# Kernel optimization log

Measured on AMD Instinct MI355X. Metric: run time of the kernel, lower is better.

## Reference

```python
import jax, jax.numpy as jnp
import numpy as np

DIM = 2048
NUM_HEADS = 16
HEAD_DIM = 128
SEQ = 4096
HDIM = NUM_HEADS * HEAD_DIM
EPS = 1e-6


def _rope_tables(seq_len, head_dim):
    quarter = head_dim // 4
    ang = (1.0 / 1024.0) ** np.linspace(0.0, 1.0, quarter, dtype=np.float32)
    ang = np.concatenate([ang, np.zeros(quarter, dtype=np.float32)])  # [head_dim//2]
    theta = np.arange(seq_len, dtype=np.float32)[:, None] * ang[None, :]  # [T, D/2]
    return jnp.asarray(np.cos(theta)), jnp.asarray(np.sin(theta))


def _rms_norm(x):
    return x * jax.lax.rsqrt(jnp.mean(x * x, axis=-1, keepdims=True) + EPS)


def _apply_rope(x, cos, sin):
    # x: [B, T, H, D]; cos/sin: [T, D/2]
    c = cos[None, :, None, :]
    s = sin[None, :, None, :]
    x1, x2 = jnp.split(x, 2, axis=-1)
    return jnp.concatenate([x1 * c + x2 * s, -x1 * s + x2 * c], axis=-1)


def setup_inputs() -> dict:
    key = jax.random.key(0)
    k1, k2, k3, k4, k5 = jax.random.split(key, 5)
    x = jax.random.normal(k1, (1, SEQ, DIM), dtype=jnp.float32)
    ve = jax.random.normal(k2, (1, SEQ, HDIM), dtype=jnp.float32)
    lambdas = jax.random.uniform(k3, (2,), dtype=jnp.float32)
    bound = (3.0 ** 0.5) * 0.5 * DIM ** (-0.5)
    qkv_w = jax.random.uniform(k4, (3, HDIM, DIM), dtype=jnp.float32, minval=-bound, maxval=bound)
    proj_w = 0.02 * jax.random.normal(k5, (DIM, HDIM), dtype=jnp.float32)
    return {"x": x, "ve": ve, "lambdas": lambdas, "qkv_w": qkv_w, "proj_w": proj_w}


def reference(x, ve, lambdas, qkv_w, proj_w):
    B, T, _ = x.shape
    cos, sin = _rope_tables(T, HEAD_DIM)
    # fused QKV projection: qkv_w [3, hdim, dim]
    qkv = jnp.einsum('btd,ced->cbte', x, qkv_w)  # [3, B, T, hdim]
    q, k, v = [a.reshape(B, T, NUM_HEADS, HEAD_DIM) for a in qkv]
    q = _apply_rope(_rms_norm(q), cos, sin)
    k = _apply_rope(_rms_norm(k), cos, sin)
    v = lambdas[0] * v + lambdas[1] * ve.reshape(v.shape)
    # causal SDPA, default scale 1/sqrt(head_dim)
    scale = 1.0 / jnp.sqrt(jnp.float32(HEAD_DIM))
    scores = jnp.einsum('bthd,bshd->bhts', q, k) * scale  # [B, H, T, T]
    causal = jnp.tril(jnp.ones((T, T), dtype=bool))
    scores = jnp.where(causal[None, None], scores, jnp.float32(-1e30))
    probs = jax.nn.softmax(scores, axis=-1)
    out = jnp.einsum('bhts,bshd->bthd', probs, v).reshape(B, T, HDIM)
    return out @ proj_w.T
```

## Files before the change

### kernel.cpp

```cpp
#include <hip/hip_runtime.h>
#include <cstdint>
#include <cstddef>

constexpr int T_SEQ = 4096;
constexpr int NH    = 16;
constexpr int HD    = 128;
constexpr int DIM   = 2048;
constexpr int HDIM  = 2048;

typedef __attribute__((ext_vector_type(8)))  short  short8;
typedef __attribute__((ext_vector_type(4)))  float  f32x4;
typedef __attribute__((ext_vector_type(16))) float  f32x16;
typedef __attribute__((ext_vector_type(8)))  unsigned short u16x8;
typedef __attribute__((ext_vector_type(4)))  unsigned short u16x4;
typedef __attribute__((ext_vector_type(4)))  unsigned uint4v;
typedef __attribute__((ext_vector_type(2)))  int int2v;

__device__ __forceinline__ unsigned short f2bf(float f) {
  unsigned u = __float_as_uint(f);
  return (unsigned short)((u + 0x7FFFu + ((u >> 16) & 1u)) >> 16);
}
__device__ __forceinline__ float bf2f(unsigned short h) {
  return __uint_as_float(((unsigned)h) << 16);
}
__device__ __forceinline__ void gload_lds16(const void* g, void* l) {
  __builtin_amdgcn_global_load_lds((const __attribute__((address_space(1))) void*)g,
                                   (__attribute__((address_space(3))) void*)l, 16, 0, 0);
}
__device__ __forceinline__ int2v plswap(int a, int b) {
  return __builtin_amdgcn_permlane32_swap(a, b, false, false);
}
__device__ __forceinline__ void bar() {
  asm volatile("" ::: "memory");
  __builtin_amdgcn_s_barrier();
  asm volatile("" ::: "memory");
}
#define VMCNT(n) asm volatile("s_waitcnt vmcnt(" #n ")" ::: "memory")

__global__ __launch_bounds__(256) void prep_all(const float* __restrict__ x,
                                                const float* __restrict__ qkv_w,
                                                const float* __restrict__ proj_w,
                                                unsigned short* __restrict__ xb,
                                                unsigned short* __restrict__ wqb,
                                                unsigned short* __restrict__ pwb,
                                                float* __restrict__ cosT,
                                                float* __restrict__ sinT) {
  constexpr int N1 = T_SEQ * DIM / 4;
  constexpr int N2 = N1 + 3 * HDIM * DIM / 4;
  constexpr int N3 = N2 + DIM * HDIM / 4;
  int gid = blockIdx.x * 256 + threadIdx.x;
  const float* src; unsigned short* dst; int i4;
  if (gid < N1)      { src = x;      dst = xb;  i4 = gid; }
  else if (gid < N2) { src = qkv_w;  dst = wqb; i4 = gid - N1; }
  else if (gid < N3) { src = proj_w; dst = pwb; i4 = gid - N2; }
  else {
    int idx = gid - N3;
    int t = idx >> 6, i = idx & 63;
    float ang = (i < 32) ? exp2f(-10.0f * (float)i / 31.0f) : 0.0f;
    float th = (float)t * ang;
    cosT[idx] = cosf(th);
    sinT[idx] = sinf(th);
    return;
  }
  float4 v = ((const float4*)src)[i4];
  u16x4 o; o.x = f2bf(v.x); o.y = f2bf(v.y); o.z = f2bf(v.z); o.w = f2bf(v.w);
  ((u16x4*)dst)[i4] = o;
}

template <int MODE>
__global__ __launch_bounds__(512) void gemm256(const unsigned short* __restrict__ A,
                                               const unsigned short* __restrict__ B,
                                               int K, unsigned short* __restrict__ outb,
                                               float* __restrict__ outf, int N) {
  __shared__ __align__(16) char SM[3 * 49152];
  const int tid = threadIdx.x, w = tid >> 6, lane = tid & 63;
  const int wm = w >> 2, wn = w & 3;
  const int lr = lane >> 4, lc = lane & 15, lc7 = lc & 7;
  const int cpx = gridDim.x >> 3;
  const int idx = (blockIdx.x & 7) * cpx + (blockIdx.x >> 3);
  const int m0 = (idx & 31) * 128, n0 = (idx >> 5) * 256;

  const int arow = lane >> 3;
  const int xcol = ((lane & 7) ^ ((lane >> 3) & 7)) * 8;

  auto stageA = [&](int buf, int t) {
    char* base = SM + buf * 49152;
#pragma unroll
    for (int i = 0; i < 2; i++) {
      int c = w + i * 8;
      gload_lds16(A + (size_t)(m0 + c * 8 + arow) * K + t * 64 + xcol, base + c * 1024);
    }
  };
  auto stageB0 = [&](int buf, int t) {
    char* base = SM + buf * 49152 + 16384;
    gload_lds16(B + (size_t)(n0 + w * 8 + arow) * K + t * 64 + xcol, base + w * 1024);
  };
  auto stageB1 = [&](int buf, int t) {
    char* base = SM + buf * 49152 + 16384;
#pragma unroll
    for (int i = 1; i < 4; i++) {
      int c = w + i * 8;
      gload_lds16(B + (size_t)(n0 + c * 8 + arow) * K + t * 64 + xcol, base + c * 1024);
    }
  };

  f32x4 acc[4][4] = {};
  const int NT = K >> 6;

  stageA(0, 0); stageB0(0, 0); stageB1(0, 0);
  stageA(1, 1); stageB0(1, 1); stageB1(1, 1);
  VMCNT(6);
  bar();

#pragma unroll 1
  for (int t = 0; t < NT; t++) {
    const int c = t % 3, s = (t + 2) % 3;
    const bool st = (t + 2) < NT;
    const char* Ab = SM + c * 49152;
    const char* Bb = Ab + 16384;

    short8 a[4], b[4];
#pragma unroll
    for (int mi = 0; mi < 4; mi++)
      a[mi] = *(const short8*)(Ab + (wm * 64 + mi * 16 + lc) * 128 + ((0 + lr) ^ lc7) * 16);
#pragma unroll
    for (int ni = 0; ni < 4; ni++)
      b[ni] = *(const short8*)(Bb + (wn * 64 + ni * 16 + lc) * 128 + ((0 + lr) ^ lc7) * 16);
    if (st) { stageA(s, t + 2); stageB0(s, t + 2); }
    bar();
    __builtin_amdgcn_s_setprio(1);
#pragma unroll
    for (int mi = 0; mi < 4; mi++)
#pragma unroll
      for (int ni = 0; ni < 4; ni++)
        acc[mi][ni] = __builtin_amdgcn_mfma_f32_16x16x32_bf16(a[mi], b[ni], acc[mi][ni], 0, 0, 0);
    __builtin_amdgcn_s_setprio(0);
    bar();

#pragma unroll
    for (int mi = 0; mi < 4; mi++)
      a[mi] = *(const short8*)(Ab + (wm * 64 + mi * 16 + lc) * 128 + ((4 + lr) ^ lc7) * 16);
#pragma unroll
    for (int ni = 0; ni < 4; ni++)
      b[ni] = *(const short8*)(Bb + (wn * 64 + ni * 16 + lc) * 128 + ((4 + lr) ^ lc7) * 16);
    if (st) stageB1(s, t + 2);
    if (st) { VMCNT(6); } else { VMCNT(0); }
    bar();
    __builtin_amdgcn_s_setprio(1);
#pragma unroll
    for (int mi = 0; mi < 4; mi++)
#pragma unroll
      for (int ni = 0; ni < 4; ni++)
        acc[mi][ni] = __builtin_amdgcn_mfma_f32_16x16x32_bf16(a[mi], b[ni], acc[mi][ni], 0, 0, 0);
    __builtin_amdgcn_s_setprio(0);
    bar();
  }

#pragma unroll
  for (int mi = 0; mi < 4; mi++)
#pragma unroll
    for (int ni = 0; ni < 4; ni++)
#pragma unroll
      for (int r = 0; r < 4; r++) {
        int t = m0 + wm * 64 + mi * 16 + lr * 4 + r;
        int n = n0 + wn * 64 + ni * 16 + lc;
        float v = acc[mi][ni][r];
        if (MODE == 0) {
          int cc = n >> 11, e = n & 2047, h = e >> 7, d = e & 127;
          outb[(((size_t)cc * NH + h) * T_SEQ + t) * HD + d] = f2bf(v);
        } else {
          outf[(size_t)t * N + n] = v;
        }
      }
}

__global__ __launch_bounds__(256) void norm_rope(unsigned short* __restrict__ qkvb,
                                                 const float* __restrict__ cosT,
                                                 const float* __restrict__ sinT) {
  const int tid = threadIdx.x;
  const int li = tid & 15;
  const int row = blockIdx.x * 16 + (tid >> 4);
  const int t = row & (T_SEQ - 1);
  unsigned short* rp = qkvb + (size_t)row * HD + li * 8;
  u16x8 raw = *(const u16x8*)rp;

  float v[8]; float ss = 0.0f;
#pragma unroll
  for (int j = 0; j < 8; j++) { v[j] = bf2f(raw[j]); ss += v[j] * v[j]; }
#pragma unroll
  for (int off = 1; off < 16; off <<= 1) ss += __shfl_xor(ss, off, 16);
  float rs = rsqrtf(ss * (1.0f / 128.0f) + 1e-6f);
  if (row < NH * T_SEQ) rs *= 0.088388347648318447f * 1.44269504f;

  uint4v rw = __builtin_bit_cast(uint4v, raw);
  uint4v pwv;
  pwv.x = (unsigned)__shfl_xor((int)rw.x, 8, 16);
  pwv.y = (unsigned)__shfl_xor((int)rw.y, 8, 16);
  pwv.z = (unsigned)__shfl_xor((int)rw.z, 8, 16);
  pwv.w = (unsigned)__shfl_xor((int)rw.w, 8, 16);
  u16x8 praw = __builtin_bit_cast(u16x8, pwv);
  float pv[8];
#pragma unroll
  for (int j = 0; j < 8; j++) pv[j] = bf2f(praw[j]);

  const int e0 = (li & 7) * 8;
  const bool hi8 = li >= 8;
  float4 c0 = *(const float4*)(cosT + t * 64 + e0);
  float4 c1 = *(const float4*)(cosT + t * 64 + e0 + 4);
  float4 s0 = *(const float4*)(sinT + t * 64 + e0);
  float4 s1 = *(const float4*)(sinT + t * 64 + e0 + 4);
  float cc[8] = {c0.x, c0.y, c0.z, c0.w, c1.x, c1.y, c1.z, c1.w};
  float sn[8] = {s0.x, s0.y, s0.z, s0.w, s1.x, s1.y, s1.z, s1.w};

  u16x8 o;
#pragma unroll
  for (int j = 0; j < 8; j++) {
    float x1 = hi8 ? pv[j] : v[j];
    float x2 = hi8 ? v[j] : pv[j];
    float r = hi8 ? (-x1 * sn[j] + x2 * cc[j]) : (x1 * cc[j] + x2 * sn[j]);
    o[j] = f2bf(r * rs);
  }
  *(u16x8*)rp = o;
}

__global__ __launch_bounds__(256) void vmix_transpose(const unsigned short* __restrict__ vb,
                                                      const float* __restrict__ ve,
                                                      const float* __restrict__ lam,
                                                      unsigned short* __restrict__ vt) {
  __shared__ float tile[64][65];
  const int h = blockIdx.z, t0 = blockIdx.x * 64, d0 = blockIdx.y * 64;
  const float l0 = lam[0], l1 = lam[1];
  const int tid = threadIdx.x;
  const int tl = tid >> 4, dl4 = (tid & 15) * 4;
#pragma unroll
  for (int i = 0; i < 4; i++) {
    int t_local = tl + i * 16;
    int t = t0 + t_local;
    const unsigned short* vp = vb + ((size_t)h * T_SEQ + t) * HD + d0 + dl4;
    const float* vep = ve + (size_t)t * HDIM + h * HD + d0 + dl4;
    u16x4 vv = *(const u16x4*)vp;
    float4 vef = *(const float4*)vep;
    tile[t_local][dl4 + 0] = l0 * bf2f(vv.x) + l1 * vef.x;
    tile[t_local][dl4 + 1] = l0 * bf2f(vv.y) + l1 * vef.y;
    tile[t_local][dl4 + 2] = l0 * bf2f(vv.z) + l1 * vef.z;
    tile[t_local][dl4 + 3] = l0 * bf2f(vv.w) + l1 * vef.w;
  }
  __syncthreads();
#pragma unroll
  for (int i = 0; i < 2; i++) {
    int idx = tid + i * 256;
    int d_local = idx >> 3, tloc = (idx & 7) * 8;
    u16x8 o;
#pragma unroll
    for (int j = 0; j < 8; j++) o[j] = f2bf(tile[tloc + j][d_local]);
    *(u16x8*)(vt + ((size_t)h * HD + d0 + d_local) * T_SEQ + t0 + tloc) = o;
  }
}

__global__ __launch_bounds__(512)
__attribute__((amdgpu_waves_per_eu(2, 2)))
void attn_fwd(const unsigned short* __restrict__ qb,
              const unsigned short* __restrict__ kb,
              const unsigned short* __restrict__ vt,
              unsigned short* __restrict__ ao) {
  __shared__ __align__(16) char SMEM[131072];
  __shared__ int gctr[2];
  const int bid = blockIdx.x;
  const int h  = (bid & 7) + ((bid >> 7) << 3);
  const int pr = (bid >> 3) & 15;
  const int tid = threadIdx.x, w = tid >> 6, lane = tid & 63;
  const int g = w >> 2, wq = w & 3;
  const int l31 = lane & 31, hi = lane >> 5, r7 = l31 & 7;
  const unsigned short* qh = qb + (size_t)h * T_SEQ * HD;
  const unsigned short* kh = kb + (size_t)h * T_SEQ * HD;
  const unsigned short* vh = vt + (size_t)h * HD * T_SEQ;

  if (tid < 2) gctr[tid] = 0;
  __syncthreads();
  int bcnt = 0;
  auto GBAR = [&]() {
    asm volatile("s_waitcnt lgkmcnt(0)" ::: "memory");
    ++bcnt;
    if (lane == 0)
      __hip_atomic_fetch_add(&gctr[g], 1, __ATOMIC_RELEASE, __HIP_MEMORY_SCOPE_WORKGROUP);
    while (__hip_atomic_load(&gctr[g], __ATOMIC_ACQUIRE, __HIP_MEMORY_SCOPE_WORKGROUP) < 4 * bcnt)
      __builtin_amdgcn_s_sleep(1);
  };

  char* Kbase = SMEM + g * 65536;
  char* Vbase = SMEM + g * 65536 + 32768;

  const int kcrow = lane >> 4, kcol16 = lane & 15;
  const int vcrow = lane >> 3, vslot0 = lane & 7;

  auto STAGE = [&](int buf, int t) {
#pragma unroll
    for (int i = 0; i < 4; i++) {
      int krow = (wq * 4 + i) * 4 + kcrow;
      int ksrc = (krow & ~12) | ((krow & 4) << 1) | ((krow & 8) >> 1);
      int kcol = (kcol16 ^ (krow & 7)) * 8;
      gload_lds16(kh + (size_t)(t * 64 + ksrc) * HD + kcol,
                  Kbase + buf * 16384 + (wq * 4 + i) * 1024);
      int vrow = (wq * 4 + i) * 8 + vcrow;
      int vcol = (vslot0 ^ (vrow & 7)) * 8;
      gload_lds16(vh + (size_t)vrow * T_SEQ + t * 64 + vcol,
                  Vbase + buf * 16384 + (wq * 4 + i) * 1024);
    }
  };

  const float FM = 16.5f;

#pragma unroll 1
  for (int which = 0; which < 2; ++which) {
    const int qt = which ? pr : (31 - pr);
    const int ng = qt + 1;
    const int q_row = qt * 128 + wq * 32 + l31;

    short8 qf[8];
#pragma unroll
    for (int dk = 0; dk < 8; dk++)
      qf[dk] = *(const short8*)(qh + (size_t)q_row * HD + dk * 16 + hi * 8);

    f32x16 accO[4] = {};
    float l_r = 0.0f;

    __syncthreads();
    STAGE(0, g);

#pragma unroll 1
    for (int it = 0; it < ng; it++) {
      const int t = 2 * it + g;
      const int cur = it & 1;
      asm volatile("s_waitcnt vmcnt(0)" ::: "memory");
      GBAR();
      if (it + 1 < ng) STAGE(cur ^ 1, t + 2);

      f32x16 accS0 = {}, accS1 = {};
      const char* Kb = Kbase + cur * 16384 + l31 * 256;
      __builtin_amdgcn_s_setprio(1);
#pragma unroll
      for (int dk = 0; dk < 8; dk++) {
        int sl = ((2 * dk + hi) ^ r7) * 16;
        short8 k0 = *(const short8*)(Kb + sl);
        short8 k1 = *(const short8*)(Kb + 32 * 256 + sl);
        accS0 = __builtin_amdgcn_mfma_f32_32x32x16_bf16(k0, qf[dk], accS0, 0, 0, 0);
        accS1 = __builtin_amdgcn_mfma_f32_32x32x16_bf16(k1, qf[dk], accS1, 0, 0, 0);
      }
      __builtin_amdgcn_s_setprio(0);

      float p[32];
      const bool need_mask = (t * 64 + 63) > (qt * 128 + wq * 32);
      if (need_mask) {
#pragma unroll
        for (int r = 0; r < 16; r++) {
          int kv0 = t * 64 + (r & 7) + 8 * hi + 16 * (r >> 3);
          p[r]      = (kv0      > q_row) ? 0.0f : exp2f(accS0[r] - FM);
          p[16 + r] = (kv0 + 32 > q_row) ? 0.0f : exp2f(accS1[r] - FM);
        }
      } else {
#pragma unroll
        for (int r = 0; r < 16; r++) {
          p[r]      = exp2f(accS0[r] - FM);
          p[16 + r] = exp2f(accS1[r] - FM);
        }
      }

      float s16[16];
#pragma unroll
      for (int i = 0; i < 16; i++) s16[i] = p[i] + p[i + 16];
#pragma unroll
      for (int st = 8; st >= 1; st >>= 1)
#pragma unroll
        for (int i = 0; i < st; i++) s16[i] += s16[i + st];
      int2v sr_ = plswap(__float_as_int(s16[0]), __float_as_int(s16[0]));
      l_r += s16[0] + __int_as_float(hi ? sr_.x : sr_.y);

      const char* Vb = Vbase + cur * 16384 + l31 * 128;
#pragma unroll
      for (int ks = 0; ks < 4; ks++) {
        uint4v pw;
#pragma unroll
        for (int w2 = 0; w2 < 4; w2++) {
          unsigned pk_;
          asm("v_cvt_pk_bf16_f32 %0, %1, %2"
              : "=v"(pk_) : "v"(p[8 * ks + 2 * w2]), "v"(p[8 * ks + 2 * w2 + 1]));
          pw[w2] = pk_;
        }
        short8 pb = __builtin_bit_cast(short8, pw);
        int sl = ((2 * ks + hi) ^ r7) * 16;
        __builtin_amdgcn_s_setprio(1);
#pragma unroll
        for (int dt = 0; dt < 4; dt++) {
          short8 vf = *(const short8*)(Vb + dt * 32 * 128 + sl);
          accO[dt] = __builtin_amdgcn_mfma_f32_32x32x16_bf16(vf, pb, accO[dt], 0, 0, 0);
        }
        __builtin_amdgcn_s_setprio(0);
      }
    }

    __syncthreads();
    float* SM_acc = (float*)(SMEM + 65536);
    float* SM_l   = (float*)SMEM;
    const int q_local = wq * 32 + l31;
    if (g == 1) {
#pragma unroll
      for (int dt = 0; dt < 4; dt++)
#pragma unroll
        for (int r = 0; r < 16; r++) {
          int d = 32 * dt + (r & 3) + 8 * (r >> 2) + 4 * hi;
          SM_acc[q_local * 128 + (d ^ l31)] = accO[dt][r];
        }
      if (hi == 0) SM_l[q_local] = l_r;
    }
    __syncthreads();
    if (g == 0) {
      float lo = SM_l[q_local];
      float inv = 1.0f / (l_r + lo);
#pragma unroll
      for (int dt = 0; dt < 4; dt++)
#pragma unroll
        for (int q4 = 0; q4 < 4; q4++) {
          int dbase = 32 * dt + 8 * q4 + 4 * hi;
          u16x4 o;
#pragma unroll
          for (int j = 0; j < 4; j++) {
            int r = q4 * 4 + j, d = dbase + j;
            float vo = SM_acc[q_local * 128 + (d ^ l31)];
            o[j] = f2bf((accO[dt][r] + vo) * inv);
          }
          *(u16x4*)(ao + (size_t)q_row * HDIM + h * HD + dbase) = o;
        }
    }
  }
}

extern "C" void kernel_launch(void* const* d_in, const int* in_sizes, int n_in,
                              void* d_out, int out_size, void* d_ws, size_t ws_size,
                              hipStream_t stream) {
  const float* x      = (const float*)d_in[0];
  const float* ve     = (const float*)d_in[1];
  const float* lam    = (const float*)d_in[2];
  const float* qkv_w  = (const float*)d_in[3];
  const float* proj_w = (const float*)d_in[4];
  float* out = (float*)d_out;

  char* p = (char*)d_ws;
  float* cosT = (float*)p;            p += (size_t)T_SEQ * 64 * 4;
  float* sinT = (float*)p;            p += (size_t)T_SEQ * 64 * 4;
  unsigned short* xb   = (unsigned short*)p; p += (size_t)T_SEQ * DIM * 2;
  unsigned short* wqb  = (unsigned short*)p; p += (size_t)3 * HDIM * DIM * 2;
  unsigned short* pwb  = (unsigned short*)p; p += (size_t)DIM * HDIM * 2;
  unsigned short* qkvb = (unsigned short*)p; p += (size_t)3 * NH * T_SEQ * HD * 2;
  unsigned short* vtb  = (unsigned short*)p; p += (size_t)NH * HD * T_SEQ * 2;
  unsigned short* aob  = (unsigned short*)p; p += (size_t)T_SEQ * HDIM * 2;

  constexpr int PREP_N = T_SEQ * DIM / 4 + 3 * HDIM * DIM / 4 + DIM * HDIM / 4 + T_SEQ * 64;
  prep_all<<<PREP_N / 256, 256, 0, stream>>>(x, qkv_w, proj_w, xb, wqb, pwb, cosT, sinT);

  gemm256<0><<<768, 512, 0, stream>>>(xb, wqb, DIM, qkvb, nullptr, 3 * HDIM);
  norm_rope<<<2 * NH * T_SEQ / 16, 256, 0, stream>>>(qkvb, cosT, sinT);
  vmix_transpose<<<dim3(T_SEQ / 64, HD / 64, NH), 256, 0, stream>>>(
      qkvb + (size_t)2 * NH * T_SEQ * HD, ve, lam, vtb);
  attn_fwd<<<256, 512, 0, stream>>>(qkvb, qkvb + (size_t)NH * T_SEQ * HD, vtb, aob);
  gemm256<1><<<256, 512, 0, stream>>>(aob, pwb, HDIM, nullptr, out, HDIM);
}
```

Baseline: 319.9 us.

## Add small-LDS double-buffered QKV GEMM and drop extra barriers in projection GEMM

Introduces a dedicated QKV projection kernel that uses a K-step of 32 with 48KB of double-buffered LDS instead of 144KB triple-buffered. The smaller LDS footprint is meant to let several workgroups share a CU and hide latency across blocks. It also removes two barriers per iteration from the output projection GEMM to cut sync overhead. Removing those barriers may open LDS read/write hazards with the triple-buffer staging.

```diff
diff --git a/kernel.cpp b/kernel.cpp
--- a/kernel.cpp
+++ b/kernel.cpp
@@ -36,6 +36,7 @@
   asm volatile("" ::: "memory");
 }
 #define VMCNT(n) asm volatile("s_waitcnt vmcnt(" #n ")" ::: "memory")
+#define LGKM0()  asm volatile("s_waitcnt lgkmcnt(0)" ::: "memory")
 
 __global__ __launch_bounds__(256) void prep_all(const float* __restrict__ x,
                                                 const float* __restrict__ qkv_w,
@@ -67,11 +68,85 @@
   ((u16x4*)dst)[i4] = o;
 }
 
-template <int MODE>
+__global__ __launch_bounds__(512) void gemmQ(const unsigned short* __restrict__ A,
+                                             const unsigned short* __restrict__ B,
+                                             unsigned short* __restrict__ outb) {
+  __shared__ __align__(16) char SM[2 * 24576];
+  const int tid = threadIdx.x, w = tid >> 6, lane = tid & 63;
+  const int wm = w >> 2, wn = w & 3;
+  const int lr = lane >> 4, lc = lane & 15;
+  const int cpx = gridDim.x >> 3;
+  const int idx = (blockIdx.x & 7) * cpx + (blockIdx.x >> 3);
+  const int m0 = (idx & 31) * 128, n0 = (idx >> 5) * 256;
+
+  const int srow = lane >> 2;
+  const int scol = ((lane & 3) ^ ((lane >> 3) & 3)) * 8;
+
+  auto stage = [&](int buf, int t) {
+    char* Abase = SM + buf * 24576;
+    char* Bbase = Abase + 8192;
+    gload_lds16(A + (size_t)(m0 + w * 16 + srow) * DIM + t * 32 + scol, Abase + w * 1024);
+#pragma unroll
+    for (int i = 0; i < 2; i++) {
+      int c = w + i * 8;
+      gload_lds16(B + (size_t)(n0 + c * 16 + srow) * DIM + t * 32 + scol, Bbase + c * 1024);
+    }
+  };
+
+  f32x4 acc[4][4] = {};
+  constexpr int NT = DIM / 32;
+
+  stage(0, 0);
+  stage(1, 1);
+
+  const int sl = (lr ^ ((lc >> 1) & 3)) * 16;
+
+#pragma unroll 1
+  for (int t = 0; t < NT; t++) {
+    const int buf = t & 1;
+    const char* Ab = SM + buf * 24576;
+    const char* Bb = Ab + 8192;
+
+    if (t < NT - 1) { VMCNT(3); } else { VMCNT(0); }
+    bar();
+
+    short8 a[4], b[4];
+#pragma unroll
+    for (int mi = 0; mi < 4; mi++)
+      a[mi] = *(const short8*)(Ab + (wm * 64 + mi * 16 + lc) * 64 + sl);
+#pragma unroll
+    for (int ni = 0; ni < 4; ni++)
+      b[ni] = *(const short8*)(Bb + (wn * 64 + ni * 16 + lc) * 64 + sl);
+    LGKM0();
+    bar();
+    if (t + 2 < NT) stage(buf, t + 2);
+
+    __builtin_amdgcn_s_setprio(1);
+#pragma unroll
+    for (int mi = 0; mi < 4; mi++)
+#pragma unroll
+      for (int ni = 0; ni < 4; ni++)
+        acc[mi][ni] = __builtin_amdgcn_mfma_f32_16x16x32_bf16(a[mi], b[ni], acc[mi][ni], 0, 0, 0);
+    __builtin_amdgcn_s_setprio(0);
+  }
+
+#pragma unroll
+  for (int mi = 0; mi < 4; mi++)
+#pragma unroll
+    for (int ni = 0; ni < 4; ni++)
+#pragma unroll
+      for (int r = 0; r < 4; r++) {
+        int t = m0 + wm * 64 + mi * 16 + lr * 4 + r;
+        int n = n0 + wn * 64 + ni * 16 + lc;
+        float v = acc[mi][ni][r];
+        int cc = n >> 11, e = n & 2047, h = e >> 7, d = e & 127;
+        outb[(((size_t)cc * NH + h) * T_SEQ + t) * HD + d] = f2bf(v);
+      }
+}
+
 __global__ __launch_bounds__(512) void gemm256(const unsigned short* __restrict__ A,
                                                const unsigned short* __restrict__ B,
-                                               int K, unsigned short* __restrict__ outb,
-                                               float* __restrict__ outf, int N) {
+                                               int K, float* __restrict__ outf, int N) {
   __shared__ __align__(16) char SM[3 * 49152];
   const int tid = threadIdx.x, w = tid >> 6, lane = tid & 63;
   const int wm = w >> 2, wn = w & 3;
@@ -127,7 +202,6 @@
     for (int ni = 0; ni < 4; ni++)
       b[ni] = *(const short8*)(Bb + (wn * 64 + ni * 16 + lc) * 128 + ((0 + lr) ^ lc7) * 16);
     if (st) { stageA(s, t + 2); stageB0(s, t + 2); }
-    bar();
     __builtin_amdgcn_s_setprio(1);
 #pragma unroll
     for (int mi = 0; mi < 4; mi++)
@@ -135,7 +209,6 @@
       for (int ni = 0; ni < 4; ni++)
         acc[mi][ni] = __builtin_amdgcn_mfma_f32_16x16x32_bf16(a[mi], b[ni], acc[mi][ni], 0, 0, 0);
     __builtin_amdgcn_s_setprio(0);
-    bar();
 
 #pragma unroll
     for (int mi = 0; mi < 4; mi++)
@@ -164,13 +237,7 @@
       for (int r = 0; r < 4; r++) {
         int t = m0 + wm * 64 + mi * 16 + lr * 4 + r;
         int n = n0 + wn * 64 + ni * 16 + lc;
-        float v = acc[mi][ni][r];
-        if (MODE == 0) {
-          int cc = n >> 11, e = n & 2047, h = e >> 7, d = e & 127;
-          outb[(((size_t)cc * NH + h) * T_SEQ + t) * HD + d] = f2bf(v);
-        } else {
-          outf[(size_t)t * N + n] = v;
-        }
+        outf[(size_t)t * N + n] = acc[mi][ni][r];
       }
 }
 
@@ -457,10 +524,10 @@
   constexpr int PREP_N = T_SEQ * DIM / 4 + 3 * HDIM * DIM / 4 + DIM * HDIM / 4 + T_SEQ * 64;
   prep_all<<<PREP_N / 256, 256, 0, stream>>>(x, qkv_w, proj_w, xb, wqb, pwb, cosT, sinT);
 
-  gemm256<0><<<768, 512, 0, stream>>>(xb, wqb, DIM, qkvb, nullptr, 3 * HDIM);
+  gemmQ<<<768, 512, 0, stream>>>(xb, wqb, qkvb);
   norm_rope<<<2 * NH * T_SEQ / 16, 256, 0, stream>>>(qkvb, cosT, sinT);
   vmix_transpose<<<dim3(T_SEQ / 64, HD / 64, NH), 256, 0, stream>>>(
       qkvb + (size_t)2 * NH * T_SEQ * HD, ve, lam, vtb);
   attn_fwd<<<256, 512, 0, stream>>>(qkvb, qkvb + (size_t)NH * T_SEQ * HD, vtb, aob);
-  gemm256<1><<<256, 512, 0, stream>>>(aob, pwb, HDIM, nullptr, out, HDIM);
-}
+  gemm256<<<256, 512, 0, stream>>>(aob, pwb, HDIM, out, HDIM);
+}
```

After: 322.9 us. About the same (+0.9%).
